# Kernel optimization log

Hardware: AMD Instinct MI355X
Metric: run time of the kernel (lower is better)

The kernel has to match this reference:

```python
import jax, jax.numpy as jnp
import numpy as np

D = 64        # input_dim (also per-head dim)
H = 8         # num_heads
L = 128       # split_length (block size)
NEG = -1e9


def _causal_mask(n):
    # additive causal mask: 0 on/below diagonal, -1e9 above
    i = jnp.arange(n)
    return jnp.where(i[:, None] >= i[None, :], 0.0, NEG).astype(jnp.float32)


def setup_inputs() -> dict:
    key = jax.random.key(0)
    ks = jax.random.split(key, 11)
    B, S = 4, 8192
    s = 1.0 / np.sqrt(D)
    inp = {
        "Q": jax.random.normal(ks[0], (B, S, D), jnp.float32),
        "K": jax.random.normal(ks[1], (B, S, D), jnp.float32),
        "V": jax.random.normal(ks[2], (B, S, D), jnp.float32),
        "WQ_w": jax.random.normal(ks[3], (H * D, D), jnp.float32) * s,
        "WQ_b": jnp.zeros((H * D,), jnp.float32),
        "WK_w": jax.random.normal(ks[4], (H * D, D), jnp.float32) * s,
        "WK_b": jnp.zeros((H * D,), jnp.float32),
        "WV_w": jax.random.normal(ks[5], (H * D, D), jnp.float32) * s,
        "WV_b": jnp.zeros((H * D,), jnp.float32),
        "W_w": jax.random.normal(ks[6], (D, H * D), jnp.float32) * (1.0 / np.sqrt(H * D)),
        "W_b": jnp.zeros((D,), jnp.float32),
    }
    return inp


def reference(Q, K, V, WQ_w, WQ_b, WK_w, WK_b, WV_w, WV_b, W_w, W_b):
    B, S, _ = Q.shape
    n = S // L  # number of blocks
    scale = 1.0 / jnp.sqrt(jnp.float32(D))

    def split(x, w, b):
        y = x @ w.T + b                              # [B,S,H*D]
        y = y.reshape(B, n, L, H, D)
        return y.transpose(0, 1, 3, 2, 4)            # [B,n,H,L,D]

    rQ = split(Q, WQ_w, WQ_b)
    rK = split(K, WK_w, WK_b)
    rV = split(V, WV_w, WV_b)

    # block-local causal attention
    s_mask = _causal_mask(L)
    Si = jnp.einsum('bnhqd,bnhkd->bnhqk', rQ, rK) * scale + s_mask
    sim = jax.nn.softmax(Si, axis=-1)
    oV = jnp.einsum('bnhqk,bnhkd->bnhqd', sim, rV)   # [B,n,H,L,D]

    # pooled global attention over blocks
    pooling = oV.mean(axis=3).transpose(0, 2, 1, 3)  # [B,H,n,D]
    g_mask = _causal_mask(n)
    g_Si = jnp.einsum('bhqd,bhkd->bhqk', pooling, pooling) * scale + g_mask
    g_sim = jax.nn.softmax(g_Si, axis=-1)
    global_att = jnp.einsum('bhqk,bhkd->bhqd', g_sim, pooling)  # [B,H,n,D]
    global_att = global_att.transpose(0, 2, 1, 3)    # [B,n,H,D]

    # broadcast-add global context to every position in the block
    oV = oV + global_att[:, :, :, None, :]           # [B,n,H,L,D]

    # merge heads then output projection
    merged = oV.transpose(0, 1, 3, 2, 4).reshape(B, S, H * D)
    out = merged @ W_w.T + W_b                       # [B,S,D]
    return out
```

## Files before the change

### kernel.cpp

```cpp
#include <hip/hip_runtime.h>
#include <stdint.h>

typedef float  v4f  __attribute__((ext_vector_type(4)));
typedef __bf16 v8bf __attribute__((ext_vector_type(8)));
typedef __bf16 v4bf __attribute__((ext_vector_type(4)));
typedef unsigned short u16;

#define NEGBIG (-1.0e9f)

static __device__ __forceinline__ uint2 pack4(v4f a){
  v4bf r;
  r[0]=(__bf16)a[0]; r[1]=(__bf16)a[1]; r[2]=(__bf16)a[2]; r[3]=(__bf16)a[3];
  return __builtin_bit_cast(uint2, r);
}
static __device__ __forceinline__ v8bf pack8(float4 a, float4 b){
  v8bf r;
  r[0]=(__bf16)a.x; r[1]=(__bf16)a.y; r[2]=(__bf16)a.z; r[3]=(__bf16)a.w;
  r[4]=(__bf16)b.x; r[5]=(__bf16)b.y; r[6]=(__bf16)b.z; r[7]=(__bf16)b.w;
  return r;
}
static __device__ __forceinline__ v4f mfma16(v8bf a, v8bf b, v4f c){
  return __builtin_amdgcn_mfma_f32_16x16x32_bf16(a, b, c, 0, 0, 0);
}

static __device__ __forceinline__ v8bf bfly(uint2 t0, uint2 t1, int srcA, int srcB, int hi){
  int a0 = __shfl((int)t0.x, srcA), a1 = __shfl((int)t0.y, srcA);
  int b0 = __shfl((int)t1.x, srcA), b1 = __shfl((int)t1.y, srcA);
  int a2 = __shfl((int)t0.x, srcB), a3 = __shfl((int)t0.y, srcB);
  int b2 = __shfl((int)t1.x, srcB), b3 = __shfl((int)t1.y, srcB);
  uint4 r;
  r.x = hi ? (unsigned)b0 : (unsigned)a0;
  r.y = hi ? (unsigned)b1 : (unsigned)a1;
  r.z = hi ? (unsigned)b2 : (unsigned)a2;
  r.w = hi ? (unsigned)b3 : (unsigned)a3;
  return __builtin_bit_cast(v8bf, r);
}

__global__ __launch_bounds__(256) void k_pre(
    const float* __restrict__ WQ, const float* __restrict__ WK,
    const float* __restrict__ WV, const float* __restrict__ Ww,
    u16* __restrict__ wq, u16* __restrict__ wk,
    u16* __restrict__ wv, u16* __restrict__ ww)
{
  const int seg = blockIdx.x >> 5;
  const int idx = ((blockIdx.x & 31)*256 + threadIdx.x)*4;
  const float* s = (seg==0) ? WQ : (seg==1) ? WK : (seg==2) ? WV : Ww;
  u16*       dst = (seg==0) ? wq : (seg==1) ? wk : (seg==2) ? wv : ww;
  float4 v = *(const float4*)(s + idx);
  v4f a; a[0]=v.x; a[1]=v.y; a[2]=v.z; a[3]=v.w;
  *(uint2*)(dst + idx) = pack4(a);
}

#define LDS_RK    0
#define LDS_VT    16384
#define LDS_WS    32768
#define LDS_WW    57344
#define LDS_POOL  73728
#define LDS_BIAS  77824
#define LDS_TOTAL 80896

__global__ __launch_bounds__(512, 4) void k_fused(
    const float* __restrict__ Q, const float* __restrict__ K, const float* __restrict__ V,
    const u16* __restrict__ wqbf, const u16* __restrict__ wkbf,
    const u16* __restrict__ wvbf, const u16* __restrict__ wwbf,
    const float* __restrict__ bQ, const float* __restrict__ bK, const float* __restrict__ bV,
    float* __restrict__ oVW, float* __restrict__ pool)
{
  extern __shared__ char lds[];

  const int bid = blockIdx.x;
  const int hg  = bid & 1;
  const int tile = bid >> 1;
  const int b = tile >> 6, nb = tile & 63;
  const int rowbase = tile * 128;
  const int tid = threadIdx.x;
  const int w = tid >> 6, l = tid & 63;
  const int l15 = l & 15, g = l >> 4;
  const int swz = (l15 & 7) << 4;
  const int srcA = ((l >> 4) & 1) * 32 + l15;
  const int srcB = srcA + 16;
  const int hi_  = l >> 5;
  const float scale = 0.125f;

  auto STAGE = [&](int hn, int wbuf){
    #pragma unroll
    for (int i = 0; i < 4; ++i){
      const int obase = w*4096 + i*1024;
      const int m   = obase >> 13;
      const int row = ((obase & 8191) >> 7) + (l >> 3);
      const int sc  = (l & 7) << 4;
      const char* src;
      int dst;
      if (m == 3){
        src = (const char*)wwbf + row*1024 + hn*128 + (sc ^ ((row & 7) << 4));
        dst = LDS_WW + wbuf*8192 + (obase - 24576);
      } else {
        const u16* basep = (m == 0) ? wqbf : (m == 1) ? wkbf : wvbf;
        src = (const char*)basep + hn*8192 + row*128 + (sc ^ ((row & 7) << 4));
        dst = LDS_WS + obase;
      }
      __builtin_amdgcn_global_load_lds(
          (const __attribute__((address_space(1))) unsigned int*)src,
          (__attribute__((address_space(3))) unsigned int*)(lds + dst),
          16, 0, 0);
    }
  };

  STAGE(hg*4, 0);

  if (tid < 192){
    const int arr = tid >> 6;
    const int idx = (tid & 63) * 4;
    const float* srcb = (arr==0) ? bQ : (arr==1) ? bK : bV;
    *(float4*)(lds + LDS_BIAS + arr*1024 + idx*4) = *(const float4*)(srcb + hg*256 + idx);
  }

  const int xrow = rowbase + w*16 + l15;
  v8bf xq[2], xk[2], xv[2];
  #pragma unroll
  for (int ks = 0; ks < 2; ++ks){
    const float* qp = Q + xrow*64 + ks*32 + g*8;
    const float* kp = K + xrow*64 + ks*32 + g*8;
    const float* vp = V + xrow*64 + ks*32 + g*8;
    xq[ks] = pack8(*(const float4*)qp, *(const float4*)(qp+4));
    xk[ks] = pack8(*(const float4*)kp, *(const float4*)(kp+4));
    xv[ks] = pack8(*(const float4*)vp, *(const float4*)(vp+4));
  }

  __syncthreads();

  v4f acc_out[4];
  #pragma unroll
  for (int mt = 0; mt < 4; ++mt){ v4f z = {0.f,0.f,0.f,0.f}; acc_out[mt] = z; }

  const int q = w*16 + l15;
  const float* bql = (const float*)(lds + LDS_BIAS);
  const float* bkl = bql + 256;
  const float* bvl = bql + 512;

  for (int hi = 0; hi < 4; ++hi){
    const int h  = hg*4 + hi;
    char* wsb = lds + LDS_WS;

    v4f aq[4], ak[4];
    #pragma unroll
    for (int mt = 0; mt < 4; ++mt){
      float4 b4 = *(const float4*)(bql + hi*64 + mt*16 + g*4);
      aq[mt][0]=b4.x; aq[mt][1]=b4.y; aq[mt][2]=b4.z; aq[mt][3]=b4.w;
      float4 c4 = *(const float4*)(bkl + hi*64 + mt*16 + g*4);
      ak[mt][0]=c4.x; ak[mt][1]=c4.y; ak[mt][2]=c4.z; ak[mt][3]=c4.w;
    }
    #pragma unroll
    for (int ks = 0; ks < 2; ++ks){
      #pragma unroll
      for (int mt = 0; mt < 4; ++mt){
        v8bf wqf = *(const v8bf*)(wsb + (mt*16 + l15)*128 + ((ks*64 + g*16) ^ swz));
        aq[mt] = mfma16(wqf, xq[ks], aq[mt]);
      }
      #pragma unroll
      for (int mt = 0; mt < 4; ++mt){
        v8bf wkf = *(const v8bf*)(wsb + 8192 + (mt*16 + l15)*128 + ((ks*64 + g*16) ^ swz));
        ak[mt] = mfma16(wkf, xk[ks], ak[mt]);
      }
    }
    uint2 pq[4];
    #pragma unroll
    for (int mt = 0; mt < 4; ++mt) pq[mt] = pack4(aq[mt]);
    v8bf qf0 = bfly(pq[0], pq[1], srcA, srcB, hi_);
    v8bf qf1 = bfly(pq[2], pq[3], srcA, srcB, hi_);
    #pragma unroll
    for (int mt = 0; mt < 4; ++mt)
      *(uint2*)(lds + LDS_RK + (w*16 + l15)*128 + ((mt*32 + g*8) ^ swz)) = pack4(ak[mt]);

    {
      v4f av[4];
      #pragma unroll
      for (int nt = 0; nt < 4; ++nt){
        float bs = bvl[hi*64 + nt*16 + l15];
        av[nt][0]=bs; av[nt][1]=bs; av[nt][2]=bs; av[nt][3]=bs;
      }
      #pragma unroll
      for (int ks = 0; ks < 2; ++ks)
        #pragma unroll
        for (int nt = 0; nt < 4; ++nt){
          v8bf wvf = *(const v8bf*)(wsb + 16384 + (nt*16 + l15)*128 + ((ks*64 + g*16) ^ swz));
          av[nt] = mfma16(xv[ks], wvf, av[nt]);
        }
      #pragma unroll
      for (int nt = 0; nt < 4; ++nt)
        *(uint2*)(lds + LDS_VT + (nt*16 + l15)*256 + ((w*32 + g*8) ^ swz)) = pack4(av[nt]);
    }

    __syncthreads();

    if (hi < 3) STAGE(h+1, (hi+1)&1);

    if (hi > 0 && tid < 64){
      const float* pr = (const float*)(lds + LDS_POOL + ((hi-1)&1)*2048);
      float s_ = 0.f;
      #pragma unroll
      for (int p = 0; p < 8; ++p) s_ += pr[p*64 + tid];
      pool[(b*8 + h-1)*4096 + nb*64 + tid] = s_ * (1.0f/128.0f);
    }

    float sum = 0.f;
    uint2 pp[8];
    __builtin_amdgcn_s_setprio(1);
    #pragma unroll
    for (int mt = 0; mt < 8; ++mt){
      if (mt > w){ uint2 z; z.x = 0u; z.y = 0u; pp[mt] = z; continue; }
      v4f s4 = {0.f,0.f,0.f,0.f};
      s4 = mfma16(*(const v8bf*)(lds + LDS_RK + (mt*16 + l15)*128 + ((0*64 + g*16) ^ swz)), qf0, s4);
      s4 = mfma16(*(const v8bf*)(lds + LDS_RK + (mt*16 + l15)*128 + ((1*64 + g*16) ^ swz)), qf1, s4);
      v4f e4;
      #pragma unroll
      for (int r = 0; r < 4; ++r){
        const int key = mt*16 + g*4 + r;
        float v_ = (key <= q) ? s4[r]*scale : NEGBIG;
        float p = __expf(v_);
        e4[r] = p;
        sum += p;
      }
      pp[mt] = pack4(e4);
    }
    __builtin_amdgcn_s_setprio(0);
    sum += __shfl_xor(sum, 16);
    sum += __shfl_xor(sum, 32);
    const float inv = 1.0f / sum;

    v4f oa[4];
    #pragma unroll
    for (int mt = 0; mt < 4; ++mt){ v4f z = {0.f,0.f,0.f,0.f}; oa[mt] = z; }
    const int WKn = (w >> 1) + 1;
    __builtin_amdgcn_s_setprio(1);
    #pragma unroll
    for (int ks = 0; ks < 4; ++ks){
      if (ks >= WKn) continue;
      v8bf pf = bfly(pp[2*ks], pp[2*ks+1], srcA, srcB, hi_);
      #pragma unroll
      for (int mt = 0; mt < 4; ++mt){
        v8bf vf = *(const v8bf*)(lds + LDS_VT + (mt*16 + l15)*256 + ((ks*64 + g*16) ^ swz));
        oa[mt] = mfma16(vf, pf, oa[mt]);
      }
    }
    __builtin_amdgcn_s_setprio(0);

    #pragma unroll
    for (int mt = 0; mt < 4; ++mt){
      oa[mt][0]*=inv; oa[mt][1]*=inv; oa[mt][2]*=inv; oa[mt][3]*=inv;
    }

    {
      float* prd = (float*)(lds + LDS_POOL + (hi&1)*2048);
      #pragma unroll
      for (int mt = 0; mt < 4; ++mt){
        v4f v = oa[mt];
        #pragma unroll
        for (int s_ = 1; s_ < 16; s_ <<= 1){
          v[0] += __shfl_xor(v[0], s_);
          v[1] += __shfl_xor(v[1], s_);
          v[2] += __shfl_xor(v[2], s_);
          v[3] += __shfl_xor(v[3], s_);
        }
        if (l15 == 0)
          *(float4*)(prd + w*64 + mt*16 + g*4) = make_float4(v[0], v[1], v[2], v[3]);
      }
    }

    uint2 po[4];
    #pragma unroll
    for (int mt = 0; mt < 4; ++mt) po[mt] = pack4(oa[mt]);
    v8bf of0 = bfly(po[0], po[1], srcA, srcB, hi_);
    v8bf of1 = bfly(po[2], po[3], srcA, srcB, hi_);
    {
      const char* wwb = lds + LDS_WW + (hi&1)*8192;
      #pragma unroll
      for (int ks = 0; ks < 2; ++ks){
        v8bf off = ks ? of1 : of0;
        #pragma unroll
        for (int mt = 0; mt < 4; ++mt){
          v8bf wf = *(const v8bf*)(wwb + (mt*16 + l15)*128 + ((ks*64 + g*16) ^ swz));
          acc_out[mt] = mfma16(wf, off, acc_out[mt]);
        }
      }
    }

    __syncthreads();
  }

  if (tid < 64){
    const float* pr = (const float*)(lds + LDS_POOL + (3&1)*2048);
    float s_ = 0.f;
    #pragma unroll
    for (int p = 0; p < 8; ++p) s_ += pr[p*64 + tid];
    pool[(b*8 + hg*4 + 3)*4096 + nb*64 + tid] = s_ * (1.0f/128.0f);
  }

  #pragma unroll
  for (int mt = 0; mt < 4; ++mt){
    float4 o;
    o.x = acc_out[mt][0]; o.y = acc_out[mt][1];
    o.z = acc_out[mt][2]; o.w = acc_out[mt][3];
    *(float4*)(oVW + hg*2097152 + (rowbase + w*16 + l15)*64 + mt*16 + g*4) = o;
  }
}

__global__ __launch_bounds__(512) void k_final(
    const float* __restrict__ oVW, const float* __restrict__ Ww, const float* __restrict__ Wb,
    const float* __restrict__ pool, float* __restrict__ out)
{
  __shared__ float prow[8][64];
  __shared__ float grow[8][64];
  __shared__ float gred[8][64];
  __shared__ float gadd[64];

  const int bid = blockIdx.x;
  const int b = bid >> 6, nb = bid & 63;
  const int rowbase = bid * 128;
  const int tid = threadIdx.x;
  const int w = tid >> 6, l = tid & 63;

  const float* pb = pool + (b*8 + w)*4096;

  float dot = 0.f;
  #pragma unroll
  for (int dd = 0; dd < 16; ++dd){
    float4 t  = *(const float4*)(pb + l*64  + dd*4);
    float4 qv = *(const float4*)(pb + nb*64 + dd*4);
    dot += t.x*qv.x + t.y*qv.y + t.z*qv.z + t.w*qv.w;
  }
  float sv = (l <= nb) ? dot*0.125f : NEGBIG;
  float mx = sv;
  #pragma unroll
  for (int s = 1; s < 64; s <<= 1) mx = fmaxf(mx, __shfl_xor(mx, s));
  float p = __expf(sv - mx);
  float sum = p;
  #pragma unroll
  for (int s = 1; s < 64; s <<= 1) sum += __shfl_xor(sum, s);
  prow[w][l] = p / sum;

  {
    float a = 0.f;
    for (int k = 0; k <= nb; ++k)
      a += prow[w][k] * pb[k*64 + l];
    grow[w][l] = a;
  }

  {
    const float* wr = Ww + l*512 + w*64;
    float c = 0.f;
    #pragma unroll
    for (int dd = 0; dd < 16; ++dd){
      float4 g4 = *(const float4*)(&grow[w][dd*4]);
      float4 w4 = *(const float4*)(wr + dd*4);
      c += g4.x*w4.x + g4.y*w4.y + g4.z*w4.z + g4.w*w4.w;
    }
    gred[w][l] = c;
  }
  __syncthreads();
  if (tid < 64){
    float s = Wb[tid];
    #pragma unroll
    for (int ph = 0; ph < 8; ++ph) s += gred[ph][tid];
    gadd[tid] = s;
  }
  __syncthreads();

  const int c4 = (tid & 15) * 4;
  float4 ga = *(const float4*)(&gadd[c4]);
  #pragma unroll
  for (int it = 0; it < 4; ++it){
    const int row = it*32 + (tid >> 4);
    const int idx = (rowbase + row)*64 + c4;
    float4 v0 = *(const float4*)(oVW + idx);
    float4 v1 = *(const float4*)(oVW + 2097152 + idx);
    float4 o;
    o.x = v0.x + v1.x + ga.x; o.y = v0.y + v1.y + ga.y;
    o.z = v0.z + v1.z + ga.z; o.w = v0.w + v1.w + ga.w;
    *(float4*)(out + idx) = o;
  }
}


extern "C" void kernel_launch(void* const* d_in, const int* in_sizes, int n_in,
                              void* d_out, int out_size, void* d_ws, size_t ws_size,
                              hipStream_t stream) {
  const float* Q   = (const float*)d_in[0];
  const float* K   = (const float*)d_in[1];
  const float* V   = (const float*)d_in[2];
  const float* WQw = (const float*)d_in[3];
  const float* WQb = (const float*)d_in[4];
  const float* WKw = (const float*)d_in[5];
  const float* WKb = (const float*)d_in[6];
  const float* WVw = (const float*)d_in[7];
  const float* WVb = (const float*)d_in[8];
  const float* Ww  = (const float*)d_in[9];
  const float* Wb  = (const float*)d_in[10];

  char* ws = (char*)d_ws;
  float* oVW  = (float*)(ws + 0);
  float* pool = (float*)(ws + 16777216);
  u16*   wqbf = (u16*)(ws + 17825792);
  u16*   wkbf = (u16*)(ws + 17891328);
  u16*   wvbf = (u16*)(ws + 17956864);
  u16*   wwbf = (u16*)(ws + 18022400);

  float* outp = (float*)d_out;

  k_pre<<<128, 256, 0, stream>>>(WQw, WKw, WVw, Ww, wqbf, wkbf, wvbf, wwbf);
  k_fused<<<512, 512, LDS_TOTAL, stream>>>(Q, K, V, wqbf, wkbf, wvbf, wwbf,
                                           WQb, WKb, WVb, oVW, pool);
  k_final<<<256, 512, 0, stream>>>(oVW, Ww, Wb, pool, outp);
}
```

Measured before the change: 80.49 us.

## Split heads into four groups per tile and read WV/WW fragments from global memory

The fused kernel now launches 1024 blocks, each handling 2 heads instead of 4, and the final kernel sums four partial output-projection slices instead of two. The WV and W_out weight fragments and the biases are read directly from global/L2 rather than staged in LDS. This shrinks the LDS footprint to raise occupancy and parallelism. The cost is more partial-sum traffic in workspace, since oVW doubles, plus uncached global loads for the weights inside the MFMA loops.

After: 93.84 us. 16.6% more time.

```diff
diff --git a/kernel.cpp b/kernel.cpp
--- a/kernel.cpp
+++ b/kernel.cpp
@@ -54,10 +54,8 @@
 #define LDS_RK    0
 #define LDS_VT    16384
 #define LDS_WS    32768
-#define LDS_WW    57344
-#define LDS_POOL  73728
-#define LDS_BIAS  77824
-#define LDS_TOTAL 80896
+#define LDS_POOL  49152
+#define LDS_TOTAL 53248
 
 __global__ __launch_bounds__(512, 4) void k_fused(
     const float* __restrict__ Q, const float* __restrict__ K, const float* __restrict__ V,
@@ -69,8 +67,8 @@
   extern __shared__ char lds[];
 
   const int bid = blockIdx.x;
-  const int hg  = bid & 1;
-  const int tile = bid >> 1;
+  const int tile = bid & 255;
+  const int hgi  = bid >> 8;
   const int b = tile >> 6, nb = tile & 63;
   const int rowbase = tile * 128;
   const int tid = threadIdx.x;
@@ -82,38 +80,23 @@
   const int hi_  = l >> 5;
   const float scale = 0.125f;
 
-  auto STAGE = [&](int hn, int wbuf){
-    #pragma unroll
-    for (int i = 0; i < 4; ++i){
-      const int obase = w*4096 + i*1024;
+  auto STAGE = [&](int hn){
+    #pragma unroll
+    for (int i = 0; i < 2; ++i){
+      const int obase = w*2048 + i*1024;
       const int m   = obase >> 13;
       const int row = ((obase & 8191) >> 7) + (l >> 3);
       const int sc  = (l & 7) << 4;
-      const char* src;
-      int dst;
-      if (m == 3){
-        src = (const char*)wwbf + row*1024 + hn*128 + (sc ^ ((row & 7) << 4));
-        dst = LDS_WW + wbuf*8192 + (obase - 24576);
-      } else {
-        const u16* basep = (m == 0) ? wqbf : (m == 1) ? wkbf : wvbf;
-        src = (const char*)basep + hn*8192 + row*128 + (sc ^ ((row & 7) << 4));
-        dst = LDS_WS + obase;
-      }
+      const u16* basep = (m == 0) ? wqbf : wkbf;
+      const char* src = (const char*)basep + hn*8192 + row*128 + (sc ^ ((row & 7) << 4));
       __builtin_amdgcn_global_load_lds(
           (const __attribute__((address_space(1))) unsigned int*)src,
-          (__attribute__((address_space(3))) unsigned int*)(lds + dst),
+          (__attribute__((address_space(3))) unsigned int*)(lds + LDS_WS + obase),
           16, 0, 0);
     }
   };
 
-  STAGE(hg*4, 0);
-
-  if (tid < 192){
-    const int arr = tid >> 6;
-    const int idx = (tid & 63) * 4;
-    const float* srcb = (arr==0) ? bQ : (arr==1) ? bK : bV;
-    *(float4*)(lds + LDS_BIAS + arr*1024 + idx*4) = *(const float4*)(srcb + hg*256 + idx);
-  }
+  STAGE(hgi*2);
 
   const int xrow = rowbase + w*16 + l15;
   v8bf xq[2], xk[2], xv[2];
@@ -134,20 +117,20 @@
   for (int mt = 0; mt < 4; ++mt){ v4f z = {0.f,0.f,0.f,0.f}; acc_out[mt] = z; }
 
   const int q = w*16 + l15;
-  const float* bql = (const float*)(lds + LDS_BIAS);
-  const float* bkl = bql + 256;
-  const float* bvl = bql + 512;
-
-  for (int hi = 0; hi < 4; ++hi){
-    const int h  = hg*4 + hi;
+  const int wfo = l15*64 + g*8;
+
+  for (int hi = 0; hi < 2; ++hi){
+    const int h  = hgi*2 + hi;
+    const int hb = h*64;
     char* wsb = lds + LDS_WS;
+    const u16* wvp = wvbf + hb*64 + wfo;
 
     v4f aq[4], ak[4];
     #pragma unroll
     for (int mt = 0; mt < 4; ++mt){
-      float4 b4 = *(const float4*)(bql + hi*64 + mt*16 + g*4);
+      float4 b4 = *(const float4*)(bQ + hb + mt*16 + g*4);
       aq[mt][0]=b4.x; aq[mt][1]=b4.y; aq[mt][2]=b4.z; aq[mt][3]=b4.w;
-      float4 c4 = *(const float4*)(bkl + hi*64 + mt*16 + g*4);
+      float4 c4 = *(const float4*)(bK + hb + mt*16 + g*4);
       ak[mt][0]=c4.x; ak[mt][1]=c4.y; ak[mt][2]=c4.z; ak[mt][3]=c4.w;
     }
     #pragma unroll
@@ -176,14 +159,14 @@
       v4f av[4];
       #pragma unroll
       for (int nt = 0; nt < 4; ++nt){
-        float bs = bvl[hi*64 + nt*16 + l15];
+        float bs = bV[hb + nt*16 + l15];
         av[nt][0]=bs; av[nt][1]=bs; av[nt][2]=bs; av[nt][3]=bs;
       }
       #pragma unroll
       for (int ks = 0; ks < 2; ++ks)
         #pragma unroll
         for (int nt = 0; nt < 4; ++nt){
-          v8bf wvf = *(const v8bf*)(wsb + 16384 + (nt*16 + l15)*128 + ((ks*64 + g*16) ^ swz));
+          v8bf wvf = *(const v8bf*)(wvp + nt*1024 + ks*32);
           av[nt] = mfma16(xv[ks], wvf, av[nt]);
         }
       #pragma unroll
@@ -193,7 +176,7 @@
 
     __syncthreads();
 
-    if (hi < 3) STAGE(h+1, (hi+1)&1);
+    if (hi < 1) STAGE(h+1);
 
     if (hi > 0 && tid < 64){
       const float* pr = (const float*)(lds + LDS_POOL + ((hi-1)&1)*2048);
@@ -272,16 +255,13 @@
     for (int mt = 0; mt < 4; ++mt) po[mt] = pack4(oa[mt]);
     v8bf of0 = bfly(po[0], po[1], srcA, srcB, hi_);
     v8bf of1 = bfly(po[2], po[3], srcA, srcB, hi_);
-    {
-      const char* wwb = lds + LDS_WW + (hi&1)*8192;
-      #pragma unroll
-      for (int ks = 0; ks < 2; ++ks){
-        v8bf off = ks ? of1 : of0;
-        #pragma unroll
-        for (int mt = 0; mt < 4; ++mt){
-          v8bf wf = *(const v8bf*)(wwb + (mt*16 + l15)*128 + ((ks*64 + g*16) ^ swz));
-          acc_out[mt] = mfma16(wf, off, acc_out[mt]);
-        }
+    #pragma unroll
+    for (int ks = 0; ks < 2; ++ks){
+      v8bf off = ks ? of1 : of0;
+      #pragma unroll
+      for (int mt = 0; mt < 4; ++mt){
+        v8bf wf = *(const v8bf*)(wwbf + (mt*16 + l15)*512 + hb + ks*32 + g*8);
+        acc_out[mt] = mfma16(wf, off, acc_out[mt]);
       }
     }
 
@@ -289,11 +269,11 @@
   }
 
   if (tid < 64){
-    const float* pr = (const float*)(lds + LDS_POOL + (3&1)*2048);
+    const float* pr = (const float*)(lds + LDS_POOL + 2048);
     float s_ = 0.f;
     #pragma unroll
     for (int p = 0; p < 8; ++p) s_ += pr[p*64 + tid];
-    pool[(b*8 + hg*4 + 3)*4096 + nb*64 + tid] = s_ * (1.0f/128.0f);
+    pool[(b*8 + hgi*2 + 1)*4096 + nb*64 + tid] = s_ * (1.0f/128.0f);
   }
 
   #pragma unroll
@@ -301,7 +281,7 @@
     float4 o;
     o.x = acc_out[mt][0]; o.y = acc_out[mt][1];
     o.z = acc_out[mt][2]; o.w = acc_out[mt][3];
-    *(float4*)(oVW + hg*2097152 + (rowbase + w*16 + l15)*64 + mt*16 + g*4) = o;
+    *(float4*)(oVW + hgi*2097152 + (rowbase + w*16 + l15)*64 + mt*16 + g*4) = o;
   }
 }
 
@@ -372,11 +352,12 @@
   for (int it = 0; it < 4; ++it){
     const int row = it*32 + (tid >> 4);
     const int idx = (rowbase + row)*64 + c4;
-    float4 v0 = *(const float4*)(oVW + idx);
-    float4 v1 = *(const float4*)(oVW + 2097152 + idx);
-    float4 o;
-    o.x = v0.x + v1.x + ga.x; o.y = v0.y + v1.y + ga.y;
-    o.z = v0.z + v1.z + ga.z; o.w = v0.w + v1.w + ga.w;
+    float4 o = ga;
+    #pragma unroll
+    for (int s = 0; s < 4; ++s){
+      float4 v = *(const float4*)(oVW + s*2097152 + idx);
+      o.x += v.x; o.y += v.y; o.z += v.z; o.w += v.w;
+    }
     *(float4*)(out + idx) = o;
   }
 }
@@ -399,16 +380,16 @@
 
   char* ws = (char*)d_ws;
   float* oVW  = (float*)(ws + 0);
-  float* pool = (float*)(ws + 16777216);
-  u16*   wqbf = (u16*)(ws + 17825792);
-  u16*   wkbf = (u16*)(ws + 17891328);
-  u16*   wvbf = (u16*)(ws + 17956864);
-  u16*   wwbf = (u16*)(ws + 18022400);
+  float* pool = (float*)(ws + 33554432);
+  u16*   wqbf = (u16*)(ws + 34078720);
+  u16*   wkbf = (u16*)(ws + 34144256);
+  u16*   wvbf = (u16*)(ws + 34209792);
+  u16*   wwbf = (u16*)(ws + 34275328);
 
   float* outp = (float*)d_out;
 
   k_pre<<<128, 256, 0, stream>>>(WQw, WKw, WVw, Ww, wqbf, wkbf, wvbf, wwbf);
-  k_fused<<<512, 512, LDS_TOTAL, stream>>>(Q, K, V, wqbf, wkbf, wvbf, wwbf,
-                                           WQb, WKb, WVb, oVW, pool);
+  k_fused<<<1024, 512, LDS_TOTAL, stream>>>(Q, K, V, wqbf, wkbf, wvbf, wwbf,
+                                            WQb, WKb, WVb, oVW, pool);
   k_final<<<256, 512, 0, stream>>>(oVW, Ww, Wb, pool, outp);
 }
```
